# Performance work log

Hardware: AMD Instinct MI355X
Metric: run time of the kernel (lower is better)

Reference implementation:

```python
import jax, jax.numpy as jnp
import numpy as np

B = 256      # graphs per batch
N = 512      # nodes per graph
FEAT = 64    # num_features
H = 64       # nhid
DEG = 16     # avg degree
RATIO = 0.5  # pooling_ratio
E = B * N * DEG


def setup_inputs() -> dict:
    key = jax.random.key(0)
    ks = jax.random.split(key, 12)
    # edges constructed within each graph via offsets
    src_loc = jax.random.randint(ks[0], (B, N * DEG), 0, N)
    dst_loc = jax.random.randint(ks[1], (B, N * DEG), 0, N)
    offs = (jnp.arange(B) * N)[:, None]
    edge_src = (src_loc + offs).reshape(-1).astype(jnp.int32)
    edge_dst = (dst_loc + offs).reshape(-1).astype(jnp.int32)
    batch = jnp.repeat(jnp.arange(B, dtype=jnp.int32), N)
    x = jax.random.normal(ks[2], (B * N, FEAT), dtype=jnp.float32)
    edge_attr = jax.random.uniform(ks[3], (E,), dtype=jnp.float32) + 0.1
    s1 = 1.0 / np.sqrt(FEAT)
    s2 = 1.0 / np.sqrt(H)
    return {
        "x": x,
        "edge_attr": edge_attr,
        "W1": jax.random.normal(ks[4], (FEAT, H), jnp.float32) * s1,
        "b1": jnp.zeros((H,), jnp.float32),
        "Wp1": jax.random.normal(ks[5], (H, 1), jnp.float32) * s2,
        "bp1": jnp.zeros((1,), jnp.float32),
        "W2": jax.random.normal(ks[6], (H, H), jnp.float32) * s2,
        "b2": jnp.zeros((H,), jnp.float32),
        "Wp2": jax.random.normal(ks[7], (H, 1), jnp.float32) * s2,
        "bp2": jnp.zeros((1,), jnp.float32),
        "edge_src": edge_src,
        "edge_dst": edge_dst,
        "batch": batch,
    }


def gcn_conv(x, W, b, src, dst, ew, n):
    """PyG GCNConv: sym-normalized weighted adjacency + self-loops (weight 1)."""
    h = x @ W                                   # [n, out]
    deg = jnp.zeros((n,), x.dtype).at[dst].add(ew) + 1.0  # self-loop adds 1
    dinv = jax.lax.rsqrt(deg)
    coef = dinv[dst] * ew * dinv[src]           # [E]
    out = jnp.zeros_like(h).at[dst].add(coef[:, None] * h[src])
    out = out + h * (1.0 / deg)[:, None]        # self-loop term: deg^-0.5 * 1 * deg^-0.5
    return out + b


def sag_pool(x, src, dst, ew, Wp, bp, n_per):
    """SAGPool: score = GCNConv(x)->1, per-graph top-k, gate by tanh(score),
    filter edges (dropped edges represented by zero weight)."""
    n = x.shape[0]
    score = gcn_conv(x, Wp, bp, src, dst, ew, n)[:, 0]   # [n]
    k = int(np.ceil(RATIO * n_per))
    _, idx = jax.lax.top_k(score.reshape(B, n_per), k)   # [B, k] local indices
    perm = (idx + (jnp.arange(B) * n_per)[:, None]).reshape(-1)
    xn = x[perm] * jnp.tanh(score[perm])[:, None]        # [B*k, H]
    newid = jnp.full((n,), -1, jnp.int32).at[perm].set(
        jnp.arange(B * k, dtype=jnp.int32))
    ns, nd = newid[src], newid[dst]
    valid = (ns >= 0) & (nd >= 0)
    ew2 = jnp.where(valid, ew, 0.0)
    ns = jnp.where(valid, ns, 0)
    nd = jnp.where(valid, nd, 0)
    return xn, ns, nd, ew2, k


def readout(x, k):
    """[gmp || gap] per graph; each graph has exactly k nodes, contiguous."""
    xg = x.reshape(B, k, -1)
    return jnp.concatenate([xg.max(axis=1), xg.mean(axis=1)], axis=1)  # [B, 2H]


def reference(x, edge_attr, W1, b1, Wp1, bp1, W2, b2, Wp2, bp2,
              edge_src, edge_dst, batch):
    n0 = x.shape[0]
    h = jax.nn.relu(gcn_conv(x, W1, b1, edge_src, edge_dst, edge_attr, n0))
    h, s1, d1, w1e, k1 = sag_pool(h, edge_src, edge_dst, edge_attr, Wp1, bp1, N)
    x1 = readout(h, k1)
    h = jax.nn.relu(gcn_conv(h, W2, b2, s1, d1, w1e, B * k1))
    h, _, _, _, k2 = sag_pool(h, s1, d1, w1e, Wp2, bp2, k1)
    x2 = readout(h, k2)
    return (x1 + x2) / 2.0
```

## Files before the change

### kernel.cpp

```cpp
#include <hip/hip_runtime.h>
#include <math.h>

#define BG   256
#define NN   512
#define EPG  (NN * 16)
#define NE   (BG * EPG)
#define N0   (BG * NN)
#define K1   256
#define N1_  (BG * K1)
#define K2   128
#define N2_  (BG * K2)

__device__ __forceinline__ float4 f4fma(float s, float4 a, float4 c) {
    c.x = fmaf(s, a.x, c.x); c.y = fmaf(s, a.y, c.y);
    c.z = fmaf(s, a.z, c.z); c.w = fmaf(s, a.w, c.w);
    return c;
}

template <int NPG, bool REMAP>
__global__ __launch_bounds__(512)
void stage_head_kernel(const int* __restrict__ esrc, const int* __restrict__ edst,
                       const float* __restrict__ eatt, const int* __restrict__ nid,
                       int2* __restrict__ pairs, int* __restrict__ rowstart,
                       int* __restrict__ rowcnt, float* __restrict__ dinv,
                       const float4* __restrict__ X4, const float4* __restrict__ W4,
                       float4* __restrict__ Y4, int nrows, int mmb) {
    __shared__ __align__(16) char smem[52224];
    if ((int)blockIdx.x < BG) {
        int2*  lpair = (int2*)smem;
        int*   cnt   = (int*)(smem + 32768);
        float* wsum  = (float*)(smem + 32768) + NPG;
        int*   scn   = (int*)(smem + 32768) + 2 * NPG;
        float* sdinv = (float*)(smem + 32768) + 3 * NPG;
        int*   wtot  = (int*)(smem + 32768) + 4 * NPG;
        int g = blockIdx.x;
        int e0 = g * EPG, nbase = g * NPG;
        for (int ii = threadIdx.x; ii < NPG; ii += 512) { cnt[ii] = 0; wsum[ii] = 0.f; }
        __syncthreads();
        const int4*   edst4 = (const int4*)(edst + e0);
        const int4*   esrc4 = (const int4*)(esrc + e0);
        const float4* eatt4 = (const float4*)(eatt + e0);
        int ed[16]; int es[16]; float ea[16];
#pragma unroll
        for (int c = 0; c < 4; ++c) {
            int ch = threadIdx.x + c * 512;
            int4   dd = edst4[ch];
            int4   ss = esrc4[ch];
            float4 ww = eatt4[ch];
            ed[c * 4 + 0] = dd.x; ed[c * 4 + 1] = dd.y; ed[c * 4 + 2] = dd.z; ed[c * 4 + 3] = dd.w;
            es[c * 4 + 0] = ss.x; es[c * 4 + 1] = ss.y; es[c * 4 + 2] = ss.z; es[c * 4 + 3] = ss.w;
            ea[c * 4 + 0] = ww.x; ea[c * 4 + 1] = ww.y; ea[c * 4 + 2] = ww.z; ea[c * 4 + 3] = ww.w;
        }
        if (REMAP) {
#pragma unroll
            for (int j = 0; j < 16; ++j) { ed[j] = nid[ed[j]]; es[j] = nid[es[j]]; }
        }
#pragma unroll
        for (int j = 0; j < 16; ++j) {
            bool valid = !REMAP || (ed[j] >= 0 && es[j] >= 0);
            if (valid) {
                int dl = ed[j] - nbase;
                atomicAdd(&cnt[dl], 1);
                atomicAdd(&wsum[dl], ea[j]);
            }
        }
        __syncthreads();
        int i = threadIdx.x;
        int lane = i & 63, wvid = i >> 6;
        int xval = (i < NPG) ? cnt[i] : 0;
        int xs = xval;
#pragma unroll
        for (int off = 1; off < 64; off <<= 1) {
            int v = __shfl_up(xs, off, 64);
            if (lane >= off) xs += v;
        }
        if (lane == 63) wtot[wvid] = xs;
        __syncthreads();
        int woff = 0, total = 0;
#pragma unroll
        for (int t = 0; t < 8; ++t) {
            int wt = wtot[t];
            if (t < wvid) woff += wt;
            total += wt;
        }
        xs += woff;
        if (i < NPG) {
            int st = xs - xval;
            rowstart[nbase + i] = e0 + st;
            rowcnt[nbase + i]   = xval;
            float di = rsqrtf(wsum[i] + 1.0f);
            dinv[nbase + i] = di;
            sdinv[i] = di;
            scn[i] = st;
        }
        __syncthreads();
        int slots[16]; float cf[16];
#pragma unroll
        for (int j = 0; j < 16; ++j) {
            bool valid = !REMAP || (ed[j] >= 0 && es[j] >= 0);
            slots[j] = -1;
            if (valid) {
                int dl = ed[j] - nbase, sl = es[j] - nbase;
                cf[j] = sdinv[dl] * ea[j] * sdinv[sl];
                slots[j] = atomicAdd(&scn[dl], 1);
            }
        }
#pragma unroll
        for (int j = 0; j < 16; ++j)
            if (slots[j] >= 0 && slots[j] < 4096)
                lpair[slots[j]] = make_int2(es[j], __float_as_int(cf[j]));
        __syncthreads();
        int n0 = total < 4096 ? total : 4096;
        for (int k = threadIdx.x; k < n0; k += 512) pairs[e0 + k] = lpair[k];
        __syncthreads();
        if (total > 4096) {
#pragma unroll
            for (int j = 0; j < 16; ++j)
                if (slots[j] >= 4096)
                    lpair[slots[j] - 4096] = make_int2(es[j], __float_as_int(cf[j]));
            __syncthreads();
            int n1 = total - 4096;
            for (int k = threadIdx.x; k < n1; k += 512) pairs[e0 + 4096 + k] = lpair[k];
        }
    } else {
        float (*sW)[68] = (float (*)[68])smem;
        int p = threadIdx.x >> 8;
        int t = threadIdx.x & 255;
        float (*sX)[68] = (float (*)[68])(smem + 17408 + p * 17408);
#pragma unroll
        for (int u = 0; u < 2; ++u) {
            int idx = threadIdx.x + u * 512;
            int r = idx >> 4, c4 = idx & 15;
            *(float4*)&sW[r][c4 * 4] = W4[idx];
        }
        int mb = blockIdx.x - BG;
        int ntiles = nrows >> 6;
        int rg = t >> 4, cg = t & 15;
        for (int tile = mb * 2 + p; tile < ntiles; tile += mmb * 2) {
            __syncthreads();
            int row0 = tile << 6;
#pragma unroll
            for (int u = 0; u < 4; ++u) {
                int idx = t + u * 256;
                int r = idx >> 4, c4 = idx & 15;
                *(float4*)&sX[r][c4 * 4] = X4[(size_t)(row0 + r) * 16 + c4];
            }
            __syncthreads();
            float4 acc0 = make_float4(0.f, 0.f, 0.f, 0.f);
            float4 acc1 = acc0, acc2 = acc0, acc3 = acc0;
#pragma unroll
            for (int k4 = 0; k4 < 16; ++k4) {
                float4 xv0 = *(const float4*)&sX[rg * 4 + 0][k4 * 4];
                float4 xv1 = *(const float4*)&sX[rg * 4 + 1][k4 * 4];
                float4 xv2 = *(const float4*)&sX[rg * 4 + 2][k4 * 4];
                float4 xv3 = *(const float4*)&sX[rg * 4 + 3][k4 * 4];
                float4 wv0 = *(const float4*)&sW[k4 * 4 + 0][cg * 4];
                float4 wv1 = *(const float4*)&sW[k4 * 4 + 1][cg * 4];
                float4 wv2 = *(const float4*)&sW[k4 * 4 + 2][cg * 4];
                float4 wv3 = *(const float4*)&sW[k4 * 4 + 3][cg * 4];
                acc0 = f4fma(xv0.x, wv0, acc0); acc0 = f4fma(xv0.y, wv1, acc0);
                acc0 = f4fma(xv0.z, wv2, acc0); acc0 = f4fma(xv0.w, wv3, acc0);
                acc1 = f4fma(xv1.x, wv0, acc1); acc1 = f4fma(xv1.y, wv1, acc1);
                acc1 = f4fma(xv1.z, wv2, acc1); acc1 = f4fma(xv1.w, wv3, acc1);
                acc2 = f4fma(xv2.x, wv0, acc2); acc2 = f4fma(xv2.y, wv1, acc2);
                acc2 = f4fma(xv2.z, wv2, acc2); acc2 = f4fma(xv2.w, wv3, acc2);
                acc3 = f4fma(xv3.x, wv0, acc3); acc3 = f4fma(xv3.y, wv1, acc3);
                acc3 = f4fma(xv3.z, wv2, acc3); acc3 = f4fma(xv3.w, wv3, acc3);
            }
            size_t ob = (size_t)(row0 + rg * 4) * 16 + cg;
            Y4[ob]      = acc0;
            Y4[ob + 16] = acc1;
            Y4[ob + 32] = acc2;
            Y4[ob + 48] = acc3;
        }
    }
}

template <int NPG>
__global__ __launch_bounds__(256)
void gather_feat_kernel(const float4* __restrict__ hx4, const int2* __restrict__ pairs,
                        const int* __restrict__ rowstart, const int* __restrict__ rowcnt,
                        const float* __restrict__ dinv, const float4* __restrict__ b4,
                        const float4* __restrict__ wp4, float* __restrict__ hp,
                        float4* __restrict__ out4) {
    constexpr int BPG = NPG / 16;
    int i   = blockIdx.x;
    int xcd = i & 7;
    int k   = i >> 3;
    int g     = xcd * (BG / 8) + k / BPG;
    int chunk = k % BPG;
    int lane16 = threadIdx.x & 15;
    int sub    = (threadIdx.x >> 4) & 3;
    int wv     = threadIdx.x >> 6;
    int lanebase = (threadIdx.x & 63) & 48;
    int node = g * NPG + chunk * 16 + wv * 4 + sub;

    float di = dinv[node];
    int st = rowstart[node], cn = rowcnt[node];
    float4 acc = hx4[(size_t)node * 16 + lane16];
    float dii = di * di;
    float4 bb = b4[lane16];
    acc.x = fmaf(acc.x, dii, bb.x);
    acc.y = fmaf(acc.y, dii, bb.y);
    acc.z = fmaf(acc.z, dii, bb.z);
    acc.w = fmaf(acc.w, dii, bb.w);

    for (int eb = 0; eb < cn; eb += 16) {
        int m = cn - eb; if (m > 16) m = 16;
        int2 pr = make_int2(0, 0);
        if (lane16 < m) pr = pairs[st + eb + lane16];
        float4 vbuf[4];
#pragma unroll
        for (int j0 = 0; j0 < 4; ++j0) {
            if (j0 < m) {
                int s = __shfl(pr.x, lanebase + j0, 64);
                vbuf[j0] = hx4[(size_t)s * 16 + lane16];
            }
        }
        for (int jb = 0; jb < m; jb += 4) {
#pragma unroll
            for (int u = 0; u < 4; ++u) {
                int j = jb + u;
                if (j < m) {
                    float c = __int_as_float(__shfl(pr.y, lanebase + j, 64));
                    float4 v = vbuf[u];
                    int jn = j + 4;
                    if (jn < m) {
                        int s = __shfl(pr.x, lanebase + jn, 64);
                        vbuf[u] = hx4[(size_t)s * 16 + lane16];
                    }
                    acc = f4fma(c, v, acc);
                }
            }
        }
    }
    acc.x = fmaxf(acc.x, 0.f); acc.y = fmaxf(acc.y, 0.f);
    acc.z = fmaxf(acc.z, 0.f); acc.w = fmaxf(acc.w, 0.f);
    out4[(size_t)node * 16 + lane16] = acc;
    float4 w4 = wp4[lane16];
    float t = acc.x * w4.x + acc.y * w4.y + acc.z * w4.z + acc.w * w4.w;
    t += __shfl_xor(t, 1, 64); t += __shfl_xor(t, 2, 64);
    t += __shfl_xor(t, 4, 64); t += __shfl_xor(t, 8, 64);
    if (lane16 == 0) hp[node] = t;
}

template <int NPG, int K, bool FINAL>
__global__ __launch_bounds__(512)
void score_pool_kernel(const float* __restrict__ hp, const int2* __restrict__ pairs,
                       const int* __restrict__ rowstart, const int* __restrict__ rowcnt,
                       const float* __restrict__ dinv, const float* __restrict__ bp,
                       const float4* __restrict__ h4, int* __restrict__ nid,
                       float4* __restrict__ xn4, float* __restrict__ xr,
                       const float* __restrict__ x1r, float* __restrict__ out) {
    __shared__ float  shp[NPG];
    __shared__ float  ssc[NPG];
    __shared__ int    lperm[K];
    __shared__ float  lgate[K];
    __shared__ float4 smx[32][16];
    __shared__ float4 ssm[32][16];
    int g = blockIdx.x, base = g * NPG;
    for (int i = threadIdx.x; i < NPG; i += 512) shp[i] = hp[base + i];
    __syncthreads();
    for (int i = threadIdx.x; i < NPG; i += 512) {
        int st = rowstart[base + i], cn = rowcnt[base + i];
        float di = dinv[base + i];
        float acc = fmaf(shp[i], di * di, bp[0]);
        for (int j = 0; j < cn; ++j) {
            int2 pr = pairs[st + j];
            acc = fmaf(__int_as_float(pr.y), shp[pr.x - base], acc);
        }
        ssc[i] = acc;
    }
    __syncthreads();
    for (int i = threadIdx.x; i < NPG; i += 512) {
        float si = ssc[i];
        int rank = 0;
        for (int j = 0; j < NPG; ++j) {
            float sj = ssc[j];
            rank += (sj > si) || (sj == si && j < i);
        }
        if (rank < K) {
            nid[base + i] = g * K + rank;
            lperm[rank]   = i;
            lgate[rank]   = tanhf(si);
        } else {
            nid[base + i] = -1;
        }
    }
    __syncthreads();
    int q16 = threadIdx.x & 15;
    int jg  = threadIdx.x >> 4;
    float4 mx = make_float4(-3.402823466e38f, -3.402823466e38f, -3.402823466e38f, -3.402823466e38f);
    float4 sm = make_float4(0.f, 0.f, 0.f, 0.f);
    for (int j = jg; j < K; j += 32) {
        float gt = lgate[j];
        float4 v = h4[(size_t)(base + lperm[j]) * 16 + q16];
        v.x *= gt; v.y *= gt; v.z *= gt; v.w *= gt;
        xn4[((size_t)g * K + j) * 16 + q16] = v;
        mx.x = fmaxf(mx.x, v.x); mx.y = fmaxf(mx.y, v.y);
        mx.z = fmaxf(mx.z, v.z); mx.w = fmaxf(mx.w, v.w);
        sm.x += v.x; sm.y += v.y; sm.z += v.z; sm.w += v.w;
    }
    smx[jg][q16] = mx; ssm[jg][q16] = sm;
    __syncthreads();
    if (jg == 0) {
#pragma unroll
        for (int t = 1; t < 32; ++t) {
            float4 a = smx[t][q16], b = ssm[t][q16];
            mx.x = fmaxf(mx.x, a.x); mx.y = fmaxf(mx.y, a.y);
            mx.z = fmaxf(mx.z, a.z); mx.w = fmaxf(mx.w, a.w);
            sm.x += b.x; sm.y += b.y; sm.z += b.z; sm.w += b.w;
        }
        float invK = 1.f / K;
        int c = q16 * 4;
        float mr[4] = {mx.x, mx.y, mx.z, mx.w};
        float ar[4] = {sm.x * invK, sm.y * invK, sm.z * invK, sm.w * invK};
#pragma unroll
        for (int u = 0; u < 4; ++u) {
            if (FINAL) {
                out[g * 128 + c + u]      = 0.5f * (x1r[g * 128 + c + u]      + mr[u]);
                out[g * 128 + 64 + c + u] = 0.5f * (x1r[g * 128 + 64 + c + u] + ar[u]);
            } else {
                xr[g * 128 + c + u]      = mr[u];
                xr[g * 128 + 64 + c + u] = ar[u];
            }
        }
    }
}

extern "C" void kernel_launch(void* const* d_in, const int* in_sizes, int n_in,
                              void* d_out, int out_size, void* d_ws, size_t ws_size,
                              hipStream_t stream) {
    const float* x    = (const float*)d_in[0];
    const float* eatt = (const float*)d_in[1];
    const float* W1   = (const float*)d_in[2];
    const float* b1   = (const float*)d_in[3];
    const float* Wp1  = (const float*)d_in[4];
    const float* bp1  = (const float*)d_in[5];
    const float* W2   = (const float*)d_in[6];
    const float* b2   = (const float*)d_in[7];
    const float* Wp2  = (const float*)d_in[8];
    const float* bp2  = (const float*)d_in[9];
    const int*   esrc = (const int*)d_in[10];
    const int*   edst = (const int*)d_in[11];
    float* out = (float*)d_out;

    float* ws = (float*)d_ws;
    size_t o = 0;
    float* A    = ws + o; o += (size_t)N0 * 64;
    float* Bb   = ws + o; o += (size_t)N0 * 64;
    int2*  prs  = (int2*)(ws + o); o += (size_t)NE * 2;
    int*   rst  = (int*)(ws + o); o += N0;
    int*   rcn  = (int*)(ws + o); o += N0;
    float* dinv = ws + o; o += N0;
    float* hp   = ws + o; o += N0;
    int*   nid  = (int*)(ws + o); o += N0;
    float* x1r  = ws + o; o += BG * 128;

    float* hx1 = A;
    float* h1  = Bb;
    float* xn1 = A;
    float* hx2 = A + (size_t)N1_ * 64;
    float* h2  = Bb;
    float* xn2 = A;

    stage_head_kernel<NN, false><<<BG + 512, 512, 0, stream>>>(
        esrc, edst, eatt, nullptr, prs, rst, rcn, dinv,
        (const float4*)x, (const float4*)W1, (float4*)hx1, N0, 512);
    gather_feat_kernel<NN><<<BG * (NN / 16), 256, 0, stream>>>(
        (const float4*)hx1, prs, rst, rcn, dinv, (const float4*)b1, (const float4*)Wp1, hp, (float4*)h1);
    score_pool_kernel<NN, K1, false><<<BG, 512, 0, stream>>>(
        hp, prs, rst, rcn, dinv, bp1, (const float4*)h1, nid, (float4*)xn1, x1r, nullptr, nullptr);
    stage_head_kernel<K1, true><<<BG + 256, 512, 0, stream>>>(
        esrc, edst, eatt, nid, prs, rst, rcn, dinv,
        (const float4*)xn1, (const float4*)W2, (float4*)hx2, N1_, 256);
    gather_feat_kernel<K1><<<BG * (K1 / 16), 256, 0, stream>>>(
        (const float4*)hx2, prs, rst, rcn, dinv, (const float4*)b2, (const float4*)Wp2, hp, (float4*)h2);
    score_pool_kernel<K1, K2, true><<<BG, 512, 0, stream>>>(
        hp, prs, rst, rcn, dinv, bp2, (const float4*)h2, nid, (float4*)xn2, nullptr, x1r, out);
}
```

Baseline: 250.2 us.

## Fuse feature gather, score conv and top-k pooling into one per-graph kernel

Replaces the separate gather_feat and score_pool kernels with a single tail kernel, one block per graph. The block stages the graph's transformed features in shared memory (padded rows) and does the neighbour aggregation from LDS instead of global gathers. Post-ReLU features and projection scores stay in registers through scoring, ranking and gating, which removes the h/hp round trips and the reloading of selected rows. The cost is 256 blocks of 512 threads with large shared memory (about 139KB at NPG=512), so occupancy and parallelism drop compared with the 8192-block gather kernel.

After: 247.2 us. About the same (-1.2%).

```diff
diff --git a/kernel.cpp b/kernel.cpp
--- a/kernel.cpp
+++ b/kernel.cpp
@@ -176,143 +176,120 @@
     }
 }
 
-template <int NPG>
-__global__ __launch_bounds__(256)
-void gather_feat_kernel(const float4* __restrict__ hx4, const int2* __restrict__ pairs,
-                        const int* __restrict__ rowstart, const int* __restrict__ rowcnt,
-                        const float* __restrict__ dinv, const float4* __restrict__ b4,
-                        const float4* __restrict__ wp4, float* __restrict__ hp,
-                        float4* __restrict__ out4) {
-    constexpr int BPG = NPG / 16;
-    int i   = blockIdx.x;
-    int xcd = i & 7;
-    int k   = i >> 3;
-    int g     = xcd * (BG / 8) + k / BPG;
-    int chunk = k % BPG;
-    int lane16 = threadIdx.x & 15;
-    int sub    = (threadIdx.x >> 4) & 3;
-    int wv     = threadIdx.x >> 6;
-    int lanebase = (threadIdx.x & 63) & 48;
-    int node = g * NPG + chunk * 16 + wv * 4 + sub;
-
-    float di = dinv[node];
-    int st = rowstart[node], cn = rowcnt[node];
-    float4 acc = hx4[(size_t)node * 16 + lane16];
-    float dii = di * di;
-    float4 bb = b4[lane16];
-    acc.x = fmaf(acc.x, dii, bb.x);
-    acc.y = fmaf(acc.y, dii, bb.y);
-    acc.z = fmaf(acc.z, dii, bb.z);
-    acc.w = fmaf(acc.w, dii, bb.w);
-
-    for (int eb = 0; eb < cn; eb += 16) {
-        int m = cn - eb; if (m > 16) m = 16;
-        int2 pr = make_int2(0, 0);
-        if (lane16 < m) pr = pairs[st + eb + lane16];
-        float4 vbuf[4];
-#pragma unroll
-        for (int j0 = 0; j0 < 4; ++j0) {
-            if (j0 < m) {
-                int s = __shfl(pr.x, lanebase + j0, 64);
-                vbuf[j0] = hx4[(size_t)s * 16 + lane16];
-            }
-        }
-        for (int jb = 0; jb < m; jb += 4) {
-#pragma unroll
-            for (int u = 0; u < 4; ++u) {
-                int j = jb + u;
-                if (j < m) {
-                    float c = __int_as_float(__shfl(pr.y, lanebase + j, 64));
-                    float4 v = vbuf[u];
-                    int jn = j + 4;
-                    if (jn < m) {
-                        int s = __shfl(pr.x, lanebase + jn, 64);
-                        vbuf[u] = hx4[(size_t)s * 16 + lane16];
-                    }
-                    acc = f4fma(c, v, acc);
-                }
-            }
-        }
-    }
-    acc.x = fmaxf(acc.x, 0.f); acc.y = fmaxf(acc.y, 0.f);
-    acc.z = fmaxf(acc.z, 0.f); acc.w = fmaxf(acc.w, 0.f);
-    out4[(size_t)node * 16 + lane16] = acc;
-    float4 w4 = wp4[lane16];
-    float t = acc.x * w4.x + acc.y * w4.y + acc.z * w4.z + acc.w * w4.w;
-    t += __shfl_xor(t, 1, 64); t += __shfl_xor(t, 2, 64);
-    t += __shfl_xor(t, 4, 64); t += __shfl_xor(t, 8, 64);
-    if (lane16 == 0) hp[node] = t;
-}
-
 template <int NPG, int K, bool FINAL>
 __global__ __launch_bounds__(512)
-void score_pool_kernel(const float* __restrict__ hp, const int2* __restrict__ pairs,
-                       const int* __restrict__ rowstart, const int* __restrict__ rowcnt,
-                       const float* __restrict__ dinv, const float* __restrict__ bp,
-                       const float4* __restrict__ h4, int* __restrict__ nid,
-                       float4* __restrict__ xn4, float* __restrict__ xr,
-                       const float* __restrict__ x1r, float* __restrict__ out) {
-    __shared__ float  shp[NPG];
-    __shared__ float  ssc[NPG];
-    __shared__ int    lperm[K];
-    __shared__ float  lgate[K];
-    __shared__ float4 smx[32][16];
-    __shared__ float4 ssm[32][16];
-    int g = blockIdx.x, base = g * NPG;
-    for (int i = threadIdx.x; i < NPG; i += 512) shp[i] = hp[base + i];
-    __syncthreads();
-    for (int i = threadIdx.x; i < NPG; i += 512) {
-        int st = rowstart[base + i], cn = rowcnt[base + i];
-        float di = dinv[base + i];
-        float acc = fmaf(shp[i], di * di, bp[0]);
+void tail_kernel(const float4* __restrict__ hx4, const int2* __restrict__ pairs,
+                 const int* __restrict__ rowstart, const int* __restrict__ rowcnt,
+                 const float* __restrict__ dinv, const float4* __restrict__ b4,
+                 const float4* __restrict__ wp4, const float* __restrict__ bp,
+                 int* __restrict__ nid, float4* __restrict__ xn4,
+                 float* __restrict__ xr, const float* __restrict__ x1r,
+                 float* __restrict__ out) {
+    constexpr int PASSES = NPG / 32;
+    __shared__ __align__(16) char smem[NPG * 68 * 4];
+    float* shx = (float*)smem;
+    float* shp = (float*)smem;
+    float* ssc = (float*)smem + NPG;
+    int*   rnk = (int*)smem + 2 * NPG;
+    float4* smx = (float4*)(smem + 3 * NPG * 4);
+    float4* ssm = smx + 32 * 16;
+
+    int g = blockIdx.x, nbase = g * NPG;
+    int t = threadIdx.x;
+    int lane16 = t & 15, sub = (t >> 4) & 3, wv = t >> 6;
+    for (int i = t; i < NPG * 16; i += 512) {
+        int r = i >> 4, c4 = i & 15;
+        *(float4*)&shx[r * 68 + c4 * 4] = hx4[(size_t)nbase * 16 + i];
+    }
+    __syncthreads();
+    float4 acc[PASSES];
+    float  hpreg[PASSES];
+    float4 bb = b4[lane16];
+    float4 w4 = wp4[lane16];
+#pragma unroll
+    for (int p = 0; p < PASSES; ++p) {
+        int nl = p * 32 + wv * 4 + sub;
+        int node = nbase + nl;
+        float di = dinv[node];
+        int st = rowstart[node], cn = rowcnt[node];
+        float dii = di * di;
+        float4 a = *(const float4*)&shx[nl * 68 + lane16 * 4];
+        a.x = fmaf(a.x, dii, bb.x);
+        a.y = fmaf(a.y, dii, bb.y);
+        a.z = fmaf(a.z, dii, bb.z);
+        a.w = fmaf(a.w, dii, bb.w);
         for (int j = 0; j < cn; ++j) {
             int2 pr = pairs[st + j];
-            acc = fmaf(__int_as_float(pr.y), shp[pr.x - base], acc);
-        }
-        ssc[i] = acc;
-    }
-    __syncthreads();
-    for (int i = threadIdx.x; i < NPG; i += 512) {
+            const float4 v = *(const float4*)&shx[(pr.x - nbase) * 68 + lane16 * 4];
+            a = f4fma(__int_as_float(pr.y), v, a);
+        }
+        a.x = fmaxf(a.x, 0.f); a.y = fmaxf(a.y, 0.f);
+        a.z = fmaxf(a.z, 0.f); a.w = fmaxf(a.w, 0.f);
+        acc[p] = a;
+        float tt = a.x * w4.x + a.y * w4.y + a.z * w4.z + a.w * w4.w;
+        tt += __shfl_xor(tt, 1, 64); tt += __shfl_xor(tt, 2, 64);
+        tt += __shfl_xor(tt, 4, 64); tt += __shfl_xor(tt, 8, 64);
+        hpreg[p] = tt;
+    }
+    __syncthreads();
+#pragma unroll
+    for (int p = 0; p < PASSES; ++p) {
+        int nl = p * 32 + wv * 4 + sub;
+        if (lane16 == 0) shp[nl] = hpreg[p];
+    }
+    __syncthreads();
+    for (int i = t; i < NPG; i += 512) {
+        int st = rowstart[nbase + i], cn = rowcnt[nbase + i];
+        float di = dinv[nbase + i];
+        float a = fmaf(shp[i], di * di, bp[0]);
+        for (int j = 0; j < cn; ++j) {
+            int2 pr = pairs[st + j];
+            a = fmaf(__int_as_float(pr.y), shp[pr.x - nbase], a);
+        }
+        ssc[i] = a;
+    }
+    __syncthreads();
+    for (int i = t; i < NPG; i += 512) {
         float si = ssc[i];
         int rank = 0;
         for (int j = 0; j < NPG; ++j) {
             float sj = ssc[j];
             rank += (sj > si) || (sj == si && j < i);
         }
-        if (rank < K) {
-            nid[base + i] = g * K + rank;
-            lperm[rank]   = i;
-            lgate[rank]   = tanhf(si);
-        } else {
-            nid[base + i] = -1;
-        }
-    }
-    __syncthreads();
-    int q16 = threadIdx.x & 15;
-    int jg  = threadIdx.x >> 4;
+        rnk[i] = rank;
+        if (!FINAL) nid[nbase + i] = (rank < K) ? (g * K + rank) : -1;
+    }
+    __syncthreads();
     float4 mx = make_float4(-3.402823466e38f, -3.402823466e38f, -3.402823466e38f, -3.402823466e38f);
     float4 sm = make_float4(0.f, 0.f, 0.f, 0.f);
-    for (int j = jg; j < K; j += 32) {
-        float gt = lgate[j];
-        float4 v = h4[(size_t)(base + lperm[j]) * 16 + q16];
-        v.x *= gt; v.y *= gt; v.z *= gt; v.w *= gt;
-        xn4[((size_t)g * K + j) * 16 + q16] = v;
-        mx.x = fmaxf(mx.x, v.x); mx.y = fmaxf(mx.y, v.y);
-        mx.z = fmaxf(mx.z, v.z); mx.w = fmaxf(mx.w, v.w);
-        sm.x += v.x; sm.y += v.y; sm.z += v.z; sm.w += v.w;
-    }
-    smx[jg][q16] = mx; ssm[jg][q16] = sm;
-    __syncthreads();
-    if (jg == 0) {
-#pragma unroll
-        for (int t = 1; t < 32; ++t) {
-            float4 a = smx[t][q16], b = ssm[t][q16];
+#pragma unroll
+    for (int p = 0; p < PASSES; ++p) {
+        int nl = p * 32 + wv * 4 + sub;
+        int r = rnk[nl];
+        if (r < K) {
+            float gt = tanhf(ssc[nl]);
+            float4 v = acc[p];
+            v.x *= gt; v.y *= gt; v.z *= gt; v.w *= gt;
+            if (!FINAL) xn4[((size_t)g * K + r) * 16 + lane16] = v;
+            mx.x = fmaxf(mx.x, v.x); mx.y = fmaxf(mx.y, v.y);
+            mx.z = fmaxf(mx.z, v.z); mx.w = fmaxf(mx.w, v.w);
+            sm.x += v.x; sm.y += v.y; sm.z += v.z; sm.w += v.w;
+        }
+    }
+    int grp = t >> 4;
+    smx[grp * 16 + lane16] = mx;
+    ssm[grp * 16 + lane16] = sm;
+    __syncthreads();
+    if (grp == 0) {
+#pragma unroll
+        for (int u = 1; u < 32; ++u) {
+            float4 a = smx[u * 16 + lane16], b = ssm[u * 16 + lane16];
             mx.x = fmaxf(mx.x, a.x); mx.y = fmaxf(mx.y, a.y);
             mx.z = fmaxf(mx.z, a.z); mx.w = fmaxf(mx.w, a.w);
             sm.x += b.x; sm.y += b.y; sm.z += b.z; sm.w += b.w;
         }
         float invK = 1.f / K;
-        int c = q16 * 4;
+        int c = lane16 * 4;
         float mr[4] = {mx.x, mx.y, mx.z, mx.w};
         float ar[4] = {sm.x * invK, sm.y * invK, sm.z * invK, sm.w * invK};
 #pragma unroll
@@ -348,34 +325,27 @@
     float* ws = (float*)d_ws;
     size_t o = 0;
     float* A    = ws + o; o += (size_t)N0 * 64;
-    float* Bb   = ws + o; o += (size_t)N0 * 64;
+    float* xn1  = ws + o; o += (size_t)N1_ * 64;
     int2*  prs  = (int2*)(ws + o); o += (size_t)NE * 2;
     int*   rst  = (int*)(ws + o); o += N0;
     int*   rcn  = (int*)(ws + o); o += N0;
     float* dinv = ws + o; o += N0;
-    float* hp   = ws + o; o += N0;
     int*   nid  = (int*)(ws + o); o += N0;
     float* x1r  = ws + o; o += BG * 128;
 
     float* hx1 = A;
-    float* h1  = Bb;
-    float* xn1 = A;
-    float* hx2 = A + (size_t)N1_ * 64;
-    float* h2  = Bb;
-    float* xn2 = A;
+    float* hx2 = A;
 
     stage_head_kernel<NN, false><<<BG + 512, 512, 0, stream>>>(
         esrc, edst, eatt, nullptr, prs, rst, rcn, dinv,
         (const float4*)x, (const float4*)W1, (float4*)hx1, N0, 512);
-    gather_feat_kernel<NN><<<BG * (NN / 16), 256, 0, stream>>>(
-        (const float4*)hx1, prs, rst, rcn, dinv, (const float4*)b1, (const float4*)Wp1, hp, (float4*)h1);
-    score_pool_kernel<NN, K1, false><<<BG, 512, 0, stream>>>(
-        hp, prs, rst, rcn, dinv, bp1, (const float4*)h1, nid, (float4*)xn1, x1r, nullptr, nullptr);
+    tail_kernel<NN, K1, false><<<BG, 512, 0, stream>>>(
+        (const float4*)hx1, prs, rst, rcn, dinv, (const float4*)b1,
+        (const float4*)Wp1, bp1, nid, (float4*)xn1, x1r, nullptr, nullptr);
     stage_head_kernel<K1, true><<<BG + 256, 512, 0, stream>>>(
         esrc, edst, eatt, nid, prs, rst, rcn, dinv,
         (const float4*)xn1, (const float4*)W2, (float4*)hx2, N1_, 256);
-    gather_feat_kernel<K1><<<BG * (K1 / 16), 256, 0, stream>>>(
-        (const float4*)hx2, prs, rst, rcn, dinv, (const float4*)b2, (const float4*)Wp2, hp, (float4*)h2);
-    score_pool_kernel<K1, K2, true><<<BG, 512, 0, stream>>>(
-        hp, prs, rst, rcn, dinv, bp2, (const float4*)h2, nid, (float4*)xn2, nullptr, x1r, out);
+    tail_kernel<K1, K2, true><<<BG, 512, 0, stream>>>(
+        (const float4*)hx2, prs, rst, rcn, dinv, (const float4*)b2,
+        (const float4*)Wp2, bp2, nullptr, nullptr, nullptr, x1r, out);
 }
```
